# Optimization experiments

Measured on AMD Instinct MI355X. Metric: run time of the kernel, lower is better.

The kernel has to match this reference:

```python
import jax, jax.numpy as jnp
import numpy as np

B, S, D = 2, 2048, 2048
H, H_KV, HD = 8, 1, 256   # attention heads, kv heads, head_dim
N_REP = H // H_KV


def setup_inputs() -> dict:
    key = jax.random.key(0)
    ks = jax.random.split(key, 8)
    std = 1.0 / np.sqrt(D)
    return {
        "hidden_states": jax.random.normal(ks[0], (B, S, D), dtype=jnp.float32),
        "attention_mask": jnp.zeros((B, 1, S, S), dtype=jnp.float32),
        "cos": jax.random.uniform(ks[1], (B, S, HD), dtype=jnp.float32),
        "sin": jax.random.uniform(ks[2], (B, S, HD), dtype=jnp.float32),
        "Wq": jax.random.normal(ks[3], (D, H * HD), dtype=jnp.float32) * std,
        "Wk": jax.random.normal(ks[4], (D, H_KV * HD), dtype=jnp.float32) * std,
        "Wv": jax.random.normal(ks[5], (D, H_KV * HD), dtype=jnp.float32) * std,
        "Wo": jax.random.normal(ks[6], (H * HD, D), dtype=jnp.float32) * std,
    }


def _rotate_half(x):
    x1, x2 = jnp.split(x, 2, axis=-1)
    return jnp.concatenate((-x2, x1), axis=-1)


def reference(hidden_states, attention_mask, cos, sin, Wq, Wk, Wv, Wo):
    b, s, _ = hidden_states.shape
    # projections -> [b, heads, s, hd]
    q = (hidden_states @ Wq).reshape(b, s, H, HD).transpose(0, 2, 1, 3)
    k = (hidden_states @ Wk).reshape(b, s, H_KV, HD).transpose(0, 2, 1, 3)
    v = (hidden_states @ Wv).reshape(b, s, H_KV, HD).transpose(0, 2, 1, 3)
    # RoPE (unsqueeze_dim=1)
    c = cos[:, None, :, :]
    sn = sin[:, None, :, :]
    q = q * c + _rotate_half(q) * sn
    k = k * c + _rotate_half(k) * sn
    # GQA: repeat kv heads
    k = jnp.repeat(k, N_REP, axis=1)
    v = jnp.repeat(v, N_REP, axis=1)
    # attention
    scores = jnp.einsum("bhqd,bhkd->bhqk", q, k) / jnp.sqrt(jnp.float32(HD))
    scores = scores + attention_mask[:, :, :, :k.shape[2]]
    attn_weights = jax.nn.softmax(scores.astype(jnp.float32), axis=-1).astype(q.dtype)
    # dropout p=0.0 -> identity
    out = jnp.einsum("bhqk,bhkd->bhqd", attn_weights, v)
    out = out.transpose(0, 2, 1, 3).reshape(b, s, H * HD)
    out = out @ Wo
    return out, attn_weights
```

## Files before the change

### kernel.cpp

```cpp
#include <hip/hip_runtime.h>
#include <hip/hip_bf16.h>

typedef float f32x4 __attribute__((ext_vector_type(4)));
typedef short short8 __attribute__((ext_vector_type(8)));
typedef unsigned int uint2v __attribute__((ext_vector_type(2)));

#define DI __device__ __forceinline__

DI unsigned short f2bf(float f) {
  unsigned int u = __float_as_uint(f);
  u += 0x7fffu + ((u >> 16) & 1u);
  return (unsigned short)(u >> 16);
}

DI unsigned int packbf(float a, float b) {
  return (unsigned int)f2bf(a) | ((unsigned int)f2bf(b) << 16);
}

DI void gload16(const unsigned short* g, unsigned short* l) {
  __builtin_amdgcn_global_load_lds((const __attribute__((address_space(1))) void*)g,
                                   (__attribute__((address_space(3))) void*)l, 16, 0, 0);
}

__global__ void cvt_bf16_kernel(const float* __restrict__ src,
                                unsigned short* __restrict__ dst, long n) {
  long i = ((long)blockIdx.x * blockDim.x + threadIdx.x) * 8;
  if (i >= n) return;
  float4 a = *(const float4*)(src + i);
  float4 b = *(const float4*)(src + i + 4);
  short8 v;
  v[0] = f2bf(a.x); v[1] = f2bf(a.y); v[2] = f2bf(a.z); v[3] = f2bf(a.w);
  v[4] = f2bf(b.x); v[5] = f2bf(b.y); v[6] = f2bf(b.z); v[7] = f2bf(b.w);
  *(short8*)(dst + i) = v;
}

__global__ void transpose_cvt_kernel(const float* __restrict__ src,
                                     unsigned short* __restrict__ dst,
                                     int ldsrc, int lddst, long sBatch, long dBatch) {
  __shared__ float tile[32][33];
  const float* s = src + (long)blockIdx.z * sBatch;
  unsigned short* d = dst + (long)blockIdx.z * dBatch;
  int c0 = blockIdx.x * 32, r0 = blockIdx.y * 32;
  int tx = threadIdx.x, ty = threadIdx.y;
#pragma unroll
  for (int k = 0; k < 4; k++)
    tile[ty + 8 * k][tx] = s[(long)(r0 + ty + 8 * k) * ldsrc + c0 + tx];
  __syncthreads();
#pragma unroll
  for (int k = 0; k < 4; k++)
    d[(long)(c0 + ty + 8 * k) * lddst + r0 + tx] = f2bf(tile[tx][ty + 8 * k]);
}

__global__ void transpose_v_kernel(const float* __restrict__ qkv,
                                   unsigned short* __restrict__ VtC) {
  __shared__ float tile[32][33];
  int b = blockIdx.z;
  int d0 = blockIdx.x * 32, s0 = blockIdx.y * 32;
  int tx = threadIdx.x, ty = threadIdx.y;
  const float* s = qkv + (long)b * 2048 * 2560 + 2304;
#pragma unroll
  for (int k = 0; k < 4; k++)
    tile[ty + 8 * k][tx] = s[(long)(s0 + ty + 8 * k) * 2560 + d0 + tx];
  __syncthreads();
  unsigned short* d = VtC + (long)b * 524288 + (long)(s0 >> 5) * 8192;
#pragma unroll
  for (int k = 0; k < 4; k++) {
    int dd = d0 + ty + 8 * k;
    d[dd * 32 + (tx ^ ((dd & 3) << 3))] = f2bf(tile[tx][ty + 8 * k]);
  }
}

__global__ void rope_kernel(const float* __restrict__ qkv, const float* __restrict__ cs,
                            const float* __restrict__ sn, unsigned short* __restrict__ Qb,
                            unsigned short* __restrict__ Ksw) {
  int bid = blockIdx.x;
  int hp = bid % 9;
  int bs = bid / 9;
  int d = threadIdx.x;
  long row = (long)bs * 2560 + hp * 256;
  float x = qkv[row + d];
  float o = (d < 128) ? -qkv[row + d + 128] : qkv[row + d - 128];
  long ci = (long)bs * 256 + d;
  float r = x * cs[ci] + o * sn[ci];
  unsigned short v = f2bf(r);
  if (hp < 8) {
    int b = bs >> 11, s = bs & 2047;
    Qb[((long)(b * 8 + hp) * 2048 + s) * 256 + d] = v;
  } else {
    Ksw[(long)bs * 256 + (d ^ ((bs & 7) << 3))] = v;
  }
}

template <bool AF32, bool CBF16>
__launch_bounds__(256)
__global__ void gemm_bt_kernel(const void* __restrict__ Av,
                               const unsigned short* __restrict__ Btg,
                               void* __restrict__ Cv,
                               int K, int lda, int ldb, int ldc,
                               int zShift, long aBatch, long bBatch, long cBatch, long cHead) {
  __shared__ unsigned short Asm_[128 * 32];
  __shared__ unsigned short Bsm_[128 * 32];
  int z = blockIdx.z;
  int zb = z >> zShift, zh = z - (zb << zShift);
  const unsigned short* Bt = Btg + (long)zb * bBatch;
  const unsigned short* A16 = (const unsigned short*)Av + (long)z * aBatch;
  const float* A32 = (const float*)Av + (long)z * aBatch;
  int m0 = blockIdx.y * 128, n0 = blockIdx.x * 128;
  int tid = threadIdx.x, w = tid >> 6, lane = tid & 63, c = lane & 15, t = lane >> 4;
  int wm = w >> 1, wn = w & 1;
  f32x4 zero4 = {0.f, 0.f, 0.f, 0.f};
  f32x4 acc[4][4];
#pragma unroll
  for (int i = 0; i < 4; i++)
#pragma unroll
    for (int j = 0; j < 4; j++) acc[i][j] = zero4;

  for (int kt = 0; kt < K; kt += 32) {
    if constexpr (!AF32) {
#pragma unroll
      for (int jj = 0; jj < 2; jj++) {
        int slot = (w * 2 + jj) * 64 + lane;
        int r = slot >> 2, g = slot & 3;
        int gs = g ^ ((r >> 1) & 3);
        gload16(A16 + (long)(m0 + r) * lda + kt + gs * 8, Asm_ + slot * 8);
      }
    } else {
#pragma unroll
      for (int jj = 0; jj < 2; jj++) {
        int slot = jj * 256 + tid;
        int r = slot >> 2, g = slot & 3;
        int gs = g ^ ((r >> 1) & 3);
        const float* p = A32 + (long)(m0 + r) * lda + kt + gs * 8;
        float4 x = *(const float4*)p;
        float4 y = *(const float4*)(p + 4);
        short8 v;
        v[0] = f2bf(x.x); v[1] = f2bf(x.y); v[2] = f2bf(x.z); v[3] = f2bf(x.w);
        v[4] = f2bf(y.x); v[5] = f2bf(y.y); v[6] = f2bf(y.z); v[7] = f2bf(y.w);
        *(short8*)(Asm_ + slot * 8) = v;
      }
    }
#pragma unroll
    for (int jj = 0; jj < 2; jj++) {
      int slot = (w * 2 + jj) * 64 + lane;
      int r = slot >> 2, g = slot & 3;
      int gs = g ^ ((r >> 1) & 3);
      gload16(Bt + (long)(n0 + r) * ldb + kt + gs * 8, Bsm_ + slot * 8);
    }
    __syncthreads();
    short8 af[4], bfg[4];
#pragma unroll
    for (int mi = 0; mi < 4; mi++) {
      int r = wm * 64 + mi * 16 + c;
      af[mi] = *(const short8*)(Asm_ + r * 32 + ((t ^ ((r >> 1) & 3)) * 8));
    }
#pragma unroll
    for (int ni = 0; ni < 4; ni++) {
      int r = wn * 64 + ni * 16 + c;
      bfg[ni] = *(const short8*)(Bsm_ + r * 32 + ((t ^ ((r >> 1) & 3)) * 8));
    }
#pragma unroll
    for (int mi = 0; mi < 4; mi++)
#pragma unroll
      for (int ni = 0; ni < 4; ni++)
        acc[mi][ni] = __builtin_amdgcn_mfma_f32_16x16x32_bf16(af[mi], bfg[ni], acc[mi][ni], 0, 0, 0);
    __syncthreads();
  }
  long cOff = (long)zb * cBatch + zh * cHead;
#pragma unroll
  for (int mi = 0; mi < 4; mi++) {
#pragma unroll
    for (int j = 0; j < 4; j++) {
      int row = m0 + wm * 64 + mi * 16 + t * 4 + j;
#pragma unroll
      for (int ni = 0; ni < 4; ni++) {
        int col = n0 + wn * 64 + ni * 16 + c;
        float v = acc[mi][ni][j];
        long idx = cOff + (long)row * ldc + col;
        if constexpr (CBF16) ((unsigned short*)Cv)[idx] = f2bf(v);
        else ((float*)Cv)[idx] = v;
      }
    }
  }
}

#define KC 32
__launch_bounds__(512, 4)
__global__ void attn_fused_kernel(const unsigned short* __restrict__ Qb,
                                  const unsigned short* __restrict__ Ksw,
                                  const unsigned short* __restrict__ VtC,
                                  const float* __restrict__ mask,
                                  float* __restrict__ attnW,
                                  unsigned short* __restrict__ attnO) {
  __shared__ unsigned short Ksm[2][KC * 256];
  __shared__ unsigned short Vsm[2][256 * KC];
  __shared__ unsigned short Pt[4][16 * 32];
  __shared__ float red[8][16];
  const int id = blockIdx.x;
  const int sw = (id & 7) * 64 + (id >> 3);
  const int qblk = sw & 31, bh = sw >> 5;
  const int b = bh >> 3;
  const int tid = threadIdx.x, w = tid >> 6, lane = tid & 63;
  const int c = lane & 15, t = lane >> 4;
  const int s = w & 3, h = w >> 2;
  const int q0 = qblk * 64 + s * 16;
  const int kh = 16 * h;
  const float scale = 0.0625f;

  short8 qf[8];
  {
    const unsigned short* Qrow = Qb + ((long)bh * 2048 + q0 + c) * 256 + t * 8;
#pragma unroll
    for (int ks = 0; ks < 8; ks++) qf[ks] = *(const short8*)(Qrow + ks * 32);
  }

  const unsigned short* Kg = Ksw + (long)b * 524288;
  const unsigned short* Vg = VtC + (long)b * 524288;
  const float* mrow = mask + (long)b * 4194304 + (long)(q0 + c) * 2048 + kh + t * 4;

  float lp = 0.f;

#pragma unroll
  for (int i = 0; i < 2; i++) {
    int slot = i * 512 + tid;
    gload16(Kg + slot * 8, Ksm[0] + slot * 8);
  }
  for (int kc = 0; kc < 64; kc++) {
    int cur = kc & 1;
    __syncthreads();
    if (kc < 63) {
      const unsigned short* src = Kg + (long)(kc + 1) * 8192;
#pragma unroll
      for (int i = 0; i < 2; i++) {
        int slot = i * 512 + tid;
        gload16(src + slot * 8, Ksm[cur ^ 1] + slot * 8);
      }
    }
    f32x4 mv = *(const f32x4*)(mrow + kc * 32);
    f32x4 a0 = {0.f, 0.f, 0.f, 0.f};
    __builtin_amdgcn_s_setprio(1);
#pragma unroll
    for (int ks = 0; ks < 8; ks++) {
      int g0 = ((ks * 4 + t) ^ (c & 7)) * 8;
      short8 kf = *(const short8*)(Ksm[cur] + (kh + c) * 256 + g0);
      a0 = __builtin_amdgcn_mfma_f32_16x16x32_bf16(kf, qf[ks], a0, 0, 0, 0);
    }
    __builtin_amdgcn_s_setprio(0);
#pragma unroll
    for (int j = 0; j < 4; j++) lp += __expf(a0[j] * scale + mv[j]);
  }
  lp += __shfl_xor(lp, 16);
  lp += __shfl_xor(lp, 32);
  if (t == 0) red[w][c] = lp;
  __syncthreads();
  float rinv = 1.0f / (red[s][c] + red[4 + s][c]);

  float* aWrow = attnW + (long)bh * 4194304 + (long)(q0 + c) * 2048 + kh + t * 4;
  unsigned short* myPt = &Pt[s][0];
  const int psw = (c & 3) << 3;
  f32x4 accO[8];
#pragma unroll
  for (int i = 0; i < 8; i++) accO[i] = (f32x4){0.f, 0.f, 0.f, 0.f};

#pragma unroll
  for (int i = 0; i < 2; i++) {
    int slot = i * 512 + tid;
    gload16(Kg + slot * 8, Ksm[0] + slot * 8);
    gload16(Vg + slot * 8, Vsm[0] + slot * 8);
  }
  for (int kc = 0; kc < 64; kc++) {
    int cur = kc & 1;
    __syncthreads();
    if (kc < 63) {
      const unsigned short* ksrc = Kg + (long)(kc + 1) * 8192;
      const unsigned short* vsrc = Vg + (long)(kc + 1) * 8192;
#pragma unroll
      for (int i = 0; i < 2; i++) {
        int slot = i * 512 + tid;
        gload16(ksrc + slot * 8, Ksm[cur ^ 1] + slot * 8);
        gload16(vsrc + slot * 8, Vsm[cur ^ 1] + slot * 8);
      }
    }
    f32x4 mv = *(const f32x4*)(mrow + kc * 32);
    f32x4 a0 = {0.f, 0.f, 0.f, 0.f};
    __builtin_amdgcn_s_setprio(1);
#pragma unroll
    for (int ks = 0; ks < 8; ks++) {
      int g0 = ((ks * 4 + t) ^ (c & 7)) * 8;
      short8 kf = *(const short8*)(Ksm[cur] + (kh + c) * 256 + g0);
      a0 = __builtin_amdgcn_mfma_f32_16x16x32_bf16(kf, qf[ks], a0, 0, 0, 0);
    }
    __builtin_amdgcn_s_setprio(0);
    f32x4 p;
#pragma unroll
    for (int j = 0; j < 4; j++) p[j] = __expf(a0[j] * scale + mv[j]) * rinv;
    *(f32x4*)(aWrow + kc * 32) = p;
    uint2v pw;
    pw[0] = packbf(p[0], p[1]); pw[1] = packbf(p[2], p[3]);
    *(uint2v*)(myPt + c * 32 + ((kh + t * 4) ^ psw)) = pw;
    asm volatile("s_waitcnt lgkmcnt(0)" ::: "memory");
    __builtin_amdgcn_s_barrier();
    __builtin_amdgcn_sched_barrier(0);
    short8 pa = *(const short8*)(myPt + c * 32 + ((t * 8) ^ psw));
    __builtin_amdgcn_s_setprio(1);
#pragma unroll
    for (int di = 0; di < 8; di++) {
      int d = (8 * h + di) * 16 + c;
      short8 vf = *(const short8*)(Vsm[cur] + d * 32 + ((t * 8) ^ psw));
      accO[di] = __builtin_amdgcn_mfma_f32_16x16x32_bf16(pa, vf, accO[di], 0, 0, 0);
    }
    __builtin_amdgcn_s_setprio(0);
  }
  long obase = ((long)b * 2048 + q0 + t * 4) * 2048 + (bh & 7) * 256 + h * 128 + c;
#pragma unroll
  for (int di = 0; di < 8; di++)
#pragma unroll
    for (int j = 0; j < 4; j++)
      attnO[obase + (long)j * 2048 + di * 16] = f2bf(accO[di][j]);
}

extern "C" void kernel_launch(void* const* d_in, const int* in_sizes, int n_in,
                              void* d_out, int out_size, void* d_ws, size_t ws_size,
                              hipStream_t stream) {
  const float* hidden = (const float*)d_in[0];
  const float* mask = (const float*)d_in[1];
  const float* cosb = (const float*)d_in[2];
  const float* sinb = (const float*)d_in[3];
  const float* Wq = (const float*)d_in[4];
  const float* Wk = (const float*)d_in[5];
  const float* Wv = (const float*)d_in[6];
  const float* Wo = (const float*)d_in[7];
  float* out = (float*)d_out;
  float* attnW = out + 8388608;

  char* ws = (char*)d_ws;
  unsigned short* hidB  = (unsigned short*)(ws + 0);
  unsigned short* WqkvT = (unsigned short*)(ws + 16777216);
  unsigned short* WoT   = (unsigned short*)(ws + 27262976);
  float*          qkv   = (float*)(ws + 35651584);
  unsigned short* Qb    = (unsigned short*)(ws + 77594624);
  unsigned short* Ksw   = (unsigned short*)(ws + 94371840);
  unsigned short* VtC   = (unsigned short*)(ws + 96468992);
  unsigned short* attnO = (unsigned short*)(ws + 98566144);

  cvt_bf16_kernel<<<4096, 256, 0, stream>>>(hidden, hidB, 8388608L);
  transpose_cvt_kernel<<<dim3(64, 64, 1), dim3(32, 8), 0, stream>>>(Wq, WqkvT, 2048, 2048, 0, 0);
  transpose_cvt_kernel<<<dim3(8, 64, 1), dim3(32, 8), 0, stream>>>(Wk, WqkvT + (long)2048 * 2048, 256, 2048, 0, 0);
  transpose_cvt_kernel<<<dim3(8, 64, 1), dim3(32, 8), 0, stream>>>(Wv, WqkvT + (long)2304 * 2048, 256, 2048, 0, 0);
  transpose_cvt_kernel<<<dim3(64, 64, 1), dim3(32, 8), 0, stream>>>(Wo, WoT, 2048, 2048, 0, 0);
  gemm_bt_kernel<false, false><<<dim3(20, 32, 1), 256, 0, stream>>>(
      hidB, WqkvT, qkv, 2048, 2048, 2048, 2560, 0, 0, 0, 0, 0);
  rope_kernel<<<36864, 256, 0, stream>>>(qkv, cosb, sinb, Qb, Ksw);
  transpose_v_kernel<<<dim3(8, 64, 2), dim3(32, 8), 0, stream>>>(qkv, VtC);
  attn_fused_kernel<<<512, 512, 0, stream>>>(Qb, Ksw, VtC, mask, attnW, attnO);
  gemm_bt_kernel<false, false><<<dim3(16, 32, 1), 256, 0, stream>>>(
      attnO, WoT, out, 2048, 2048, 2048, 2048, 0, 0, 0, 0, 0);
}
```

Before: 389.5 us.

## Split attention row-sum pass into separate kernel with key-split parallelism

Moves the softmax denominator (sum of exps) pass out of the fused attention kernel into its own kernel. That kernel splits the key range in two, so it launches 1024 blocks with higher launch-bounds occupancy, and writes partial sums to workspace. The second kernel reads and combines the partial sums, then computes normalized weights and P·V. This aims to expose more parallelism in the first pass, at the cost of an extra launch, recomputing the Q loads, and reusing the qkv workspace region, which is dead by then, for the partials.

```diff
diff --git a/kernel.cpp b/kernel.cpp
--- a/kernel.cpp
+++ b/kernel.cpp
@@ -184,17 +184,84 @@
 }
 
 #define KC 32
+__launch_bounds__(512, 8)
+__global__ void attn_pass1_kernel(const unsigned short* __restrict__ Qb,
+                                  const unsigned short* __restrict__ Ksw,
+                                  const float* __restrict__ mask,
+                                  float* __restrict__ lpP) {
+  __shared__ unsigned short Ksm[2][KC * 256];
+  __shared__ float red[8][16];
+  const int id = blockIdx.x;
+  const int sw = (id & 7) * 128 + (id >> 3);
+  const int ks = sw & 1, qblk = (sw >> 1) & 31, bh = sw >> 6;
+  const int b = bh >> 3;
+  const int tid = threadIdx.x, w = tid >> 6, lane = tid & 63;
+  const int c = lane & 15, t = lane >> 4;
+  const int s = w & 3, h = w >> 2;
+  const int q0 = qblk * 64 + s * 16;
+  const int kh = 16 * h;
+  const float scale = 0.0625f;
+
+  short8 qf[8];
+  {
+    const unsigned short* Qrow = Qb + ((long)bh * 2048 + q0 + c) * 256 + t * 8;
+#pragma unroll
+    for (int k = 0; k < 8; k++) qf[k] = *(const short8*)(Qrow + k * 32);
+  }
+  const unsigned short* Kg = Ksw + (long)b * 524288;
+  const float* mrow = mask + (long)b * 4194304 + (long)(q0 + c) * 2048 + kh + t * 4;
+
+  float lp = 0.f;
+  const int kc0 = ks * 32;
+#pragma unroll
+  for (int i = 0; i < 2; i++) {
+    int slot = i * 512 + tid;
+    gload16(Kg + (long)kc0 * 8192 + slot * 8, Ksm[0] + slot * 8);
+  }
+  for (int kc = 0; kc < 32; kc++) {
+    int kcg = kc0 + kc;
+    int cur = kc & 1;
+    __syncthreads();
+    if (kc < 31) {
+      const unsigned short* src = Kg + (long)(kcg + 1) * 8192;
+#pragma unroll
+      for (int i = 0; i < 2; i++) {
+        int slot = i * 512 + tid;
+        gload16(src + slot * 8, Ksm[cur ^ 1] + slot * 8);
+      }
+    }
+    f32x4 mv = *(const f32x4*)(mrow + kcg * 32);
+    f32x4 a0 = {0.f, 0.f, 0.f, 0.f};
+    __builtin_amdgcn_s_setprio(1);
+#pragma unroll
+    for (int kk = 0; kk < 8; kk++) {
+      int g0 = ((kk * 4 + t) ^ (c & 7)) * 8;
+      short8 kf = *(const short8*)(Ksm[cur] + (kh + c) * 256 + g0);
+      a0 = __builtin_amdgcn_mfma_f32_16x16x32_bf16(kf, qf[kk], a0, 0, 0, 0);
+    }
+    __builtin_amdgcn_s_setprio(0);
+#pragma unroll
+    for (int j = 0; j < 4; j++) lp += __expf(a0[j] * scale + mv[j]);
+  }
+  lp += __shfl_xor(lp, 16);
+  lp += __shfl_xor(lp, 32);
+  if (t == 0) red[w][c] = lp;
+  __syncthreads();
+  if (h == 0 && t == 0)
+    lpP[((long)bh * 2048 + q0 + c) * 2 + ks] = red[s][c] + red[4 + s][c];
+}
+
 __launch_bounds__(512, 4)
-__global__ void attn_fused_kernel(const unsigned short* __restrict__ Qb,
+__global__ void attn_pass2_kernel(const unsigned short* __restrict__ Qb,
                                   const unsigned short* __restrict__ Ksw,
                                   const unsigned short* __restrict__ VtC,
                                   const float* __restrict__ mask,
+                                  const float* __restrict__ lpP,
                                   float* __restrict__ attnW,
                                   unsigned short* __restrict__ attnO) {
   __shared__ unsigned short Ksm[2][KC * 256];
   __shared__ unsigned short Vsm[2][256 * KC];
   __shared__ unsigned short Pt[4][16 * 32];
-  __shared__ float red[8][16];
   const int id = blockIdx.x;
   const int sw = (id & 7) * 64 + (id >> 3);
   const int qblk = sw & 31, bh = sw >> 5;
@@ -210,49 +277,15 @@
   {
     const unsigned short* Qrow = Qb + ((long)bh * 2048 + q0 + c) * 256 + t * 8;
 #pragma unroll
-    for (int ks = 0; ks < 8; ks++) qf[ks] = *(const short8*)(Qrow + ks * 32);
+    for (int kk = 0; kk < 8; kk++) qf[kk] = *(const short8*)(Qrow + kk * 32);
   }
 
   const unsigned short* Kg = Ksw + (long)b * 524288;
   const unsigned short* Vg = VtC + (long)b * 524288;
   const float* mrow = mask + (long)b * 4194304 + (long)(q0 + c) * 2048 + kh + t * 4;
 
-  float lp = 0.f;
-
-#pragma unroll
-  for (int i = 0; i < 2; i++) {
-    int slot = i * 512 + tid;
-    gload16(Kg + slot * 8, Ksm[0] + slot * 8);
-  }
-  for (int kc = 0; kc < 64; kc++) {
-    int cur = kc & 1;
-    __syncthreads();
-    if (kc < 63) {
-      const unsigned short* src = Kg + (long)(kc + 1) * 8192;
-#pragma unroll
-      for (int i = 0; i < 2; i++) {
-        int slot = i * 512 + tid;
-        gload16(src + slot * 8, Ksm[cur ^ 1] + slot * 8);
-      }
-    }
-    f32x4 mv = *(const f32x4*)(mrow + kc * 32);
-    f32x4 a0 = {0.f, 0.f, 0.f, 0.f};
-    __builtin_amdgcn_s_setprio(1);
-#pragma unroll
-    for (int ks = 0; ks < 8; ks++) {
-      int g0 = ((ks * 4 + t) ^ (c & 7)) * 8;
-      short8 kf = *(const short8*)(Ksm[cur] + (kh + c) * 256 + g0);
-      a0 = __builtin_amdgcn_mfma_f32_16x16x32_bf16(kf, qf[ks], a0, 0, 0, 0);
-    }
-    __builtin_amdgcn_s_setprio(0);
-#pragma unroll
-    for (int j = 0; j < 4; j++) lp += __expf(a0[j] * scale + mv[j]);
-  }
-  lp += __shfl_xor(lp, 16);
-  lp += __shfl_xor(lp, 32);
-  if (t == 0) red[w][c] = lp;
-  __syncthreads();
-  float rinv = 1.0f / (red[s][c] + red[4 + s][c]);
+  float2 lps = *(const float2*)(lpP + ((long)bh * 2048 + q0 + c) * 2);
+  float rinv = 1.0f / (lps.x + lps.y);
 
   float* aWrow = attnW + (long)bh * 4194304 + (long)(q0 + c) * 2048 + kh + t * 4;
   unsigned short* myPt = &Pt[s][0];
@@ -284,10 +317,10 @@
     f32x4 a0 = {0.f, 0.f, 0.f, 0.f};
     __builtin_amdgcn_s_setprio(1);
 #pragma unroll
-    for (int ks = 0; ks < 8; ks++) {
-      int g0 = ((ks * 4 + t) ^ (c & 7)) * 8;
+    for (int kk = 0; kk < 8; kk++) {
+      int g0 = ((kk * 4 + t) ^ (c & 7)) * 8;
       short8 kf = *(const short8*)(Ksm[cur] + (kh + c) * 256 + g0);
-      a0 = __builtin_amdgcn_mfma_f32_16x16x32_bf16(kf, qf[ks], a0, 0, 0, 0);
+      a0 = __builtin_amdgcn_mfma_f32_16x16x32_bf16(kf, qf[kk], a0, 0, 0, 0);
     }
     __builtin_amdgcn_s_setprio(0);
     f32x4 p;
@@ -337,6 +370,7 @@
   unsigned short* WqkvT = (unsigned short*)(ws + 16777216);
   unsigned short* WoT   = (unsigned short*)(ws + 27262976);
   float*          qkv   = (float*)(ws + 35651584);
+  float*          lpP   = (float*)(ws + 35651584);
   unsigned short* Qb    = (unsigned short*)(ws + 77594624);
   unsigned short* Ksw   = (unsigned short*)(ws + 94371840);
   unsigned short* VtC   = (unsigned short*)(ws + 96468992);
@@ -351,7 +385,8 @@
       hidB, WqkvT, qkv, 2048, 2048, 2048, 2560, 0, 0, 0, 0, 0);
   rope_kernel<<<36864, 256, 0, stream>>>(qkv, cosb, sinb, Qb, Ksw);
   transpose_v_kernel<<<dim3(8, 64, 2), dim3(32, 8), 0, stream>>>(qkv, VtC);
-  attn_fused_kernel<<<512, 512, 0, stream>>>(Qb, Ksw, VtC, mask, attnW, attnO);
+  attn_pass1_kernel<<<1024, 512, 0, stream>>>(Qb, Ksw, mask, lpP);
+  attn_pass2_kernel<<<512, 512, 0, stream>>>(Qb, Ksw, VtC, mask, lpP, attnW, attnO);
   gemm_bt_kernel<false, false><<<dim3(16, 32, 1), 256, 0, stream>>>(
       attnO, WoT, out, 2048, 2048, 2048, 2048, 0, 0, 0, 0, 0);
 }
```

Measured after the change: 414.0 us. 1.06x slower.
